# Kernel tuning notes

Measured on AMD Instinct MI355X. Metric: run time of the kernel, lower is better.

## Reference

```python
import jax, jax.numpy as jnp
import numpy as np

N = 50000      # nodes
E = 800000     # edges (before self loops)
H = 4          # heads
C_IN = 128     # input feature dim
C_HID = 64     # per-head out channels (hidden_dim == output_dim)
SLOPE = 0.2    # GATConv leaky_relu negative slope


def setup_inputs() -> dict:
    key = jax.random.key(0)
    ks = jax.random.split(key, 16)
    x = jax.random.normal(ks[0], (N, C_IN), jnp.float32)
    edge_index = jax.random.randint(ks[1], (2, E), 0, N, jnp.int32)

    def p(k, shape):
        return jax.random.normal(k, shape, jnp.float32) * 0.05

    inp = {"x": x, "edge_index": edge_index}
    in_dims = [C_IN, C_HID, C_HID]
    for i in range(3):
        inp[f"W{i+1}"] = p(ks[2 + 4 * i], (in_dims[i], H * C_HID))
        inp[f"asrc{i+1}"] = p(ks[3 + 4 * i], (H, C_HID))
        inp[f"adst{i+1}"] = p(ks[4 + 4 * i], (H, C_HID))
        inp[f"b{i+1}"] = jnp.zeros((C_HID,), jnp.float32)
    return inp


def _gat_layer(x, src, dst, W, a_s, a_d, b):
    # x: [N, F_in]; src/dst: [E'] (self loops included)
    n = x.shape[0]
    h = (x @ W).reshape(n, H, -1)                      # [N, H, C]
    alpha_src = jnp.einsum('nhc,hc->nh', h, a_s)       # att_src . h  (source side)
    alpha_dst = jnp.einsum('nhc,hc->nh', h, a_d)       # att_dst . h  (target side)
    e = jax.nn.leaky_relu(alpha_src[src] + alpha_dst[dst], SLOPE)  # [E', H]
    # scatter-softmax over incoming edges of each dst node
    m = jax.ops.segment_max(e, dst, num_segments=n)    # [N, H]
    ex = jnp.exp(e - m[dst])
    denom = jax.ops.segment_sum(ex, dst, num_segments=n)
    alpha = ex / (denom[dst] + 1e-16)                  # [E', H]
    # scatter-add aggregation of weighted source features
    out = jax.ops.segment_sum(alpha[:, :, None] * h[src], dst, num_segments=n)  # [N, H, C]
    return out.mean(axis=1) + b                        # concat=False -> head mean, + bias


def reference(x, edge_index, W1, asrc1, adst1, b1, W2, asrc2, adst2, b2,
              W3, asrc3, adst3, b3):
    n = x.shape[0]
    loops = jnp.arange(n, dtype=edge_index.dtype)      # GATConv add_self_loops=True
    src = jnp.concatenate([edge_index[0], loops])
    dst = jnp.concatenate([edge_index[1], loops])
    for W, a_s, a_d, b in ((W1, asrc1, adst1, b1),
                           (W2, asrc2, adst2, b2),
                           (W3, asrc3, adst3, b3)):
        x = jax.nn.relu(_gat_layer(x, src, dst, W, a_s, a_d, b))
    return x
```

## Files before the change

### kernel.cpp

```cpp
#include <hip/hip_runtime.h>
#include <hip/hip_bf16.h>
#include <cstddef>

#define NH 4
#define CHID 64
#define HC 256

typedef __attribute__((ext_vector_type(8))) short bf16x8;
typedef __attribute__((ext_vector_type(4))) float f32x4;


__global__ void hist_kernel(const int* __restrict__ ei, int E, int N,
                            int* __restrict__ deg) {
  int i = blockIdx.x * blockDim.x + threadIdx.x;
  int EP = E + N;
  if (i >= EP) return;
  int d = (i < E) ? ei[E + i] : (i - E);
  atomicAdd(&deg[d], 1);
}

__global__ __launch_bounds__(256) void partial_sum_kernel(const int* __restrict__ deg,
                                                          int* __restrict__ part, int n) {
  __shared__ int red[4];
  int t = threadIdx.x;
  int i = blockIdx.x * 256 + t;
  int v = (i < n) ? deg[i] : 0;
#pragma unroll
  for (int o = 32; o; o >>= 1) v += __shfl_xor(v, o, 64);
  if ((t & 63) == 0) red[t >> 6] = v;
  __syncthreads();
  if (t == 0) part[blockIdx.x] = red[0] + red[1] + red[2] + red[3];
}

__global__ __launch_bounds__(256) void scan_part_kernel(int* __restrict__ part, int nb,
                                                        int* __restrict__ row_off, int n) {
  __shared__ int s[256];
  int t = threadIdx.x;
  int v = (t < nb) ? part[t] : 0;
  s[t] = v;
  __syncthreads();
  for (int o = 1; o < 256; o <<= 1) {
    int u = (t >= o) ? s[t - o] : 0;
    __syncthreads();
    s[t] += u;
    __syncthreads();
  }
  if (t < nb) part[t] = s[t] - v;
  if (t == 255) row_off[n] = s[255];
}

__global__ __launch_bounds__(256) void row_off_kernel(const int* __restrict__ deg,
                                                      const int* __restrict__ part,
                                                      int* __restrict__ row_off, int n) {
  __shared__ int s[256];
  int t = threadIdx.x;
  int i = blockIdx.x * 256 + t;
  int v = (i < n) ? deg[i] : 0;
  s[t] = v;
  __syncthreads();
  for (int o = 1; o < 256; o <<= 1) {
    int u = (t >= o) ? s[t - o] : 0;
    __syncthreads();
    s[t] += u;
    __syncthreads();
  }
  if (i < n) row_off[i] = part[blockIdx.x] + s[t] - v;
}

__global__ void scatter_kernel(const int* __restrict__ ei, int E, int N,
                               const int* __restrict__ row_off,
                               int* __restrict__ cursor, int* __restrict__ ssrc) {
  int i = blockIdx.x * blockDim.x + threadIdx.x;
  int EP = E + N;
  if (i >= EP) {
    if (i < EP + 8) ssrc[i] = 0;
    return;
  }
  int s, d;
  if (i < E) { s = ei[i]; d = ei[E + i]; } else { s = i - E; d = s; }
  int pos = row_off[d] + atomicAdd(&cursor[d], 1);
  ssrc[pos] = s;
}


__global__ void prep_kernel(const float* __restrict__ x,
                            __hip_bfloat16* __restrict__ xb, int n4,
                            const float* __restrict__ W1, const float* __restrict__ W2,
                            const float* __restrict__ W3,
                            __hip_bfloat16* __restrict__ w1b,
                            __hip_bfloat16* __restrict__ w2b,
                            __hip_bfloat16* __restrict__ w3b) {
  int i = blockIdx.x * blockDim.x + threadIdx.x;
  if (i < n4) {
    float4 v = reinterpret_cast<const float4*>(x)[i];
    __hip_bfloat16 h[4] = {__float2bfloat16(v.x), __float2bfloat16(v.y),
                           __float2bfloat16(v.z), __float2bfloat16(v.w)};
    reinterpret_cast<uint2*>(xb)[i] = *reinterpret_cast<uint2*>(h);
    return;
  }
  int j = i - n4;
  if (j >= 65536) return;
  const float* W; __hip_bfloat16* wb; int K, base;
  if (j < 32768)      { W = W1; wb = w1b; K = 128; base = j; }
  else if (j < 49152) { W = W2; wb = w2b; K = 64;  base = j - 32768; }
  else                { W = W3; wb = w3b; K = 64;  base = j - 49152; }
  int k = base >> 8;
  int c = base & 255;
  wb[c * K + k] = __float2bfloat16(W[base]);
}


template <int K>
__global__ __launch_bounds__(256) void gemm_mfma_kernel(
    const __hip_bfloat16* __restrict__ Ab,
    const __hip_bfloat16* __restrict__ Btb,
    const float* __restrict__ a_s, const float* __restrict__ a_d,
    __hip_bfloat16* __restrict__ h, float* __restrict__ asrc_n,
    float* __restrict__ adst_n, int n_rows, int row_groups) {
  extern __shared__ char smem[];
  uint4* lds4 = reinterpret_cast<uint4*>(smem);
  constexpr int KS = K / 32;
  constexpr int S16 = (128 * K * 2) >> 4;
  constexpr int rowshift = (K == 128) ? 4 : 3;
  int ch = blockIdx.y;
  int colbase = ch * 128;

  {
    const uint4* g = reinterpret_cast<const uint4*>(Btb + (size_t)colbase * K);
    for (int c = threadIdx.x; c < S16; c += 256) {
      int row = c >> rowshift;
      lds4[c ^ (row & 7)] = g[c];
    }
  }
  __syncthreads();

  int wave = threadIdx.x >> 6;
  int lane = threadIdx.x & 63;
  int n16  = lane & 15;
  int g4   = lane >> 4;
  const bf16x8 z8 = {0, 0, 0, 0, 0, 0, 0, 0};

  for (int gg = blockIdx.x; gg < row_groups; gg += gridDim.x) {
    int row0 = gg * 64 + wave * 16;
    int xrow = row0 + n16;
    bool aval = xrow < n_rows;
    size_t xbase = (size_t)xrow * K + g4 * 8;

    bf16x8 xh[KS];
#pragma unroll
    for (int s = 0; s < KS; ++s)
      xh[s] = aval ? *reinterpret_cast<const bf16x8*>(&Ab[xbase + s * 32]) : z8;

    f32x4 acc[8];
#pragma unroll
    for (int ct = 0; ct < 8; ++ct) acc[ct] = (f32x4){0.f, 0.f, 0.f, 0.f};

#pragma unroll
    for (int ct = 0; ct < 8; ++ct) {
      int wrow = ct * 16 + n16;
#pragma unroll
      for (int s = 0; s < KS; ++s) {
        int ci = ((wrow * K + s * 32 + g4 * 8) >> 3) ^ (wrow & 7);
        bf16x8 wh = *reinterpret_cast<const bf16x8*>(&lds4[ci]);
        acc[ct] = __builtin_amdgcn_mfma_f32_16x16x32_bf16(wh, xh[s], acc[ct], 0, 0, 0);
      }
    }

    int r = row0 + n16;
    bool valid = r < n_rows;

    if (valid) {
#pragma unroll
      for (int ct = 0; ct < 8; ++ct) {
        unsigned short u[4];
#pragma unroll
        for (int i = 0; i < 4; ++i) {
          __hip_bfloat16 b = __float2bfloat16(acc[ct][i]);
          u[i] = *reinterpret_cast<unsigned short*>(&b);
        }
        *reinterpret_cast<uint2*>(&h[(size_t)r * HC + colbase + ct * 16 + g4 * 4]) =
            *reinterpret_cast<uint2*>(u);
      }
    }

    float ps[2] = {0.f, 0.f};
    float pd[2] = {0.f, 0.f};
#pragma unroll
    for (int ct = 0; ct < 8; ++ct) {
      int hh = ct >> 2;
      int col = colbase + ct * 16 + g4 * 4;
      float4 as4 = *reinterpret_cast<const float4*>(&a_s[col]);
      float4 ad4 = *reinterpret_cast<const float4*>(&a_d[col]);
      ps[hh] += acc[ct][0] * as4.x + acc[ct][1] * as4.y + acc[ct][2] * as4.z + acc[ct][3] * as4.w;
      pd[hh] += acc[ct][0] * ad4.x + acc[ct][1] * ad4.y + acc[ct][2] * ad4.z + acc[ct][3] * ad4.w;
    }
#pragma unroll
    for (int hh = 0; hh < 2; ++hh) {
      ps[hh] += __shfl_xor(ps[hh], 16, 64);
      ps[hh] += __shfl_xor(ps[hh], 32, 64);
      pd[hh] += __shfl_xor(pd[hh], 16, 64);
      pd[hh] += __shfl_xor(pd[hh], 32, 64);
    }
    if (lane < 16 && valid) {
      *reinterpret_cast<float2*>(&asrc_n[(size_t)r * NH + ch * 2]) =
          make_float2(ps[0], ps[1]);
      *reinterpret_cast<float2*>(&adst_n[(size_t)r * NH + ch * 2]) =
          make_float2(pd[0], pd[1]);
    }
  }
}


__global__ __launch_bounds__(256) void aggregate_kernel(
    const int* __restrict__ row_off, const int* __restrict__ ssrc,
    const __hip_bfloat16* __restrict__ h, const float* __restrict__ asrc_n,
    const float* __restrict__ adst_n, const float* __restrict__ bias,
    __hip_bfloat16* __restrict__ out_bf, float* __restrict__ out_f32, int n_nodes) {
  int n = (blockIdx.x * blockDim.x + threadIdx.x) >> 6;
  if (n >= n_nodes) return;
  int l    = threadIdx.x & 63;
  int slot = l >> 3;
  int cp   = l & 7;
  const char* hbase = reinterpret_cast<const char*>(h);
  const float4 z4 = make_float4(0.f, 0.f, 0.f, 0.f);
  const uint4 zu = {0, 0, 0, 0};

  int beg  = row_off[n];
  int deg  = row_off[n + 1] - beg;
  float4 adn = reinterpret_cast<const float4*>(adst_n)[n];

  float facc[32];
#pragma unroll
  for (int u = 0; u < 32; ++u) facc[u] = 0.f;
  float4 ds = z4;

  auto LOADE = [&](int j, float4& a4, float& msk, uint4* d) {
    int jj  = j + slot;
    int idx = beg + jj;
    int sv  = ssrc[idx];
    a4  = reinterpret_cast<const float4*>(asrc_n)[sv];
    msk = (jj < deg) ? 1.f : 0.f;
    const char* hp = hbase + (size_t)sv * 512 + cp * 16;
    d[0] = *reinterpret_cast<const uint4*>(hp);
    d[1] = *reinterpret_cast<const uint4*>(hp + 128);
    d[2] = *reinterpret_cast<const uint4*>(hp + 256);
    d[3] = *reinterpret_cast<const uint4*>(hp + 384);
  };

  auto PROC = [&](const float4& a4, float msk, const uint4* d) {
    float e0 = a4.x + adn.x; e0 = fmaxf(e0, 0.2f * e0);
    float e1 = a4.y + adn.y; e1 = fmaxf(e1, 0.2f * e1);
    float e2 = a4.z + adn.z; e2 = fmaxf(e2, 0.2f * e2);
    float e3 = a4.w + adn.w; e3 = fmaxf(e3, 0.2f * e3);
    float w0 = __expf(e0) * msk;
    float w1 = __expf(e1) * msk;
    float w2 = __expf(e2) * msk;
    float w3 = __expf(e3) * msk;
    ds.x += w0; ds.y += w1; ds.z += w2; ds.w += w3;
#pragma unroll
    for (int hh = 0; hh < 4; ++hh) {
      float w = (hh == 0) ? w0 : (hh == 1) ? w1 : (hh == 2) ? w2 : w3;
      uint4 dd = d[hh];
      facc[hh * 8 + 0] += w * __uint_as_float(dd.x << 16);
      facc[hh * 8 + 1] += w * __uint_as_float(dd.x & 0xffff0000u);
      facc[hh * 8 + 2] += w * __uint_as_float(dd.y << 16);
      facc[hh * 8 + 3] += w * __uint_as_float(dd.y & 0xffff0000u);
      facc[hh * 8 + 4] += w * __uint_as_float(dd.z << 16);
      facc[hh * 8 + 5] += w * __uint_as_float(dd.z & 0xffff0000u);
      facc[hh * 8 + 6] += w * __uint_as_float(dd.w << 16);
      facc[hh * 8 + 7] += w * __uint_as_float(dd.w & 0xffff0000u);
    }
  };

  float4 aA = z4, aB = z4;
  float mA = 0.f, mB = 0.f;
  uint4 dA[4] = {zu, zu, zu, zu};
  uint4 dB[4] = {zu, zu, zu, zu};

  LOADE(0, aA, mA, dA);
  for (int j = 0; j < deg; j += 16) {
    if (j + 8 < deg) LOADE(j + 8, aB, mB, dB); else mB = 0.f;
    PROC(aA, mA, dA);
    if (j + 16 < deg) LOADE(j + 16, aA, mA, dA); else mA = 0.f;
    PROC(aB, mB, dB);
  }

#pragma unroll
  for (int o = 8; o <= 32; o <<= 1) {
    ds.x += __shfl_xor(ds.x, o, 64);
    ds.y += __shfl_xor(ds.y, o, 64);
    ds.z += __shfl_xor(ds.z, o, 64);
    ds.w += __shfl_xor(ds.w, o, 64);
  }
  float iv0 = 1.f / (ds.x + 1e-16f);
  float iv1 = 1.f / (ds.y + 1e-16f);
  float iv2 = 1.f / (ds.z + 1e-16f);
  float iv3 = 1.f / (ds.w + 1e-16f);

  float v[8];
#pragma unroll
  for (int u = 0; u < 8; ++u)
    v[u] = facc[u] * iv0 + facc[8 + u] * iv1 + facc[16 + u] * iv2 + facc[24 + u] * iv3;

#pragma unroll
  for (int u = 0; u < 8; ++u) {
    v[u] += __shfl_xor(v[u], 8, 64);
    v[u] += __shfl_xor(v[u], 16, 64);
    v[u] += __shfl_xor(v[u], 32, 64);
  }

  if (slot < 2) {
    float o0 = (slot == 0) ? v[0] : v[4];
    float o1 = (slot == 0) ? v[1] : v[5];
    float o2 = (slot == 0) ? v[2] : v[6];
    float o3 = (slot == 0) ? v[3] : v[7];
    int chn = cp * 8 + slot * 4;
    float4 b4 = *reinterpret_cast<const float4*>(&bias[chn]);
    o0 = fmaxf(0.25f * o0 + b4.x, 0.f);
    o1 = fmaxf(0.25f * o1 + b4.y, 0.f);
    o2 = fmaxf(0.25f * o2 + b4.z, 0.f);
    o3 = fmaxf(0.25f * o3 + b4.w, 0.f);
    if (out_f32) {
      *reinterpret_cast<float4*>(&out_f32[(size_t)n * CHID + chn]) =
          make_float4(o0, o1, o2, o3);
    } else {
      float of[4] = {o0, o1, o2, o3};
      unsigned short b16[4];
#pragma unroll
      for (int u = 0; u < 4; ++u) {
        __hip_bfloat16 bh = __float2bfloat16(of[u]);
        b16[u] = *reinterpret_cast<unsigned short*>(&bh);
      }
      *reinterpret_cast<uint2*>(&out_bf[(size_t)n * CHID + chn]) =
          *reinterpret_cast<uint2*>(b16);
    }
  }
}


extern "C" void kernel_launch(void* const* d_in, const int* in_sizes, int n_in,
                              void* d_out, int out_size, void* d_ws, size_t ws_size,
                              hipStream_t stream) {
  const float* x   = (const float*)d_in[0];
  const int*   ei  = (const int*)d_in[1];
  const float* W1  = (const float*)d_in[2];
  const float* as1 = (const float*)d_in[3];
  const float* ad1 = (const float*)d_in[4];
  const float* b1  = (const float*)d_in[5];
  const float* W2  = (const float*)d_in[6];
  const float* as2 = (const float*)d_in[7];
  const float* ad2 = (const float*)d_in[8];
  const float* b2  = (const float*)d_in[9];
  const float* W3  = (const float*)d_in[10];
  const float* as3 = (const float*)d_in[11];
  const float* ad3 = (const float*)d_in[12];
  const float* b3  = (const float*)d_in[13];

  int N  = in_sizes[0] / 128;
  int E  = in_sizes[1] / 2;
  int EP = E + N;
  int NB = (N + 255) / 256;

  __hip_bfloat16* h    = (__hip_bfloat16*)d_ws;
  __hip_bfloat16* x1b  = h + (size_t)N * HC;
  __hip_bfloat16* xb   = x1b + (size_t)N * 128;
  __hip_bfloat16* w1b  = xb + (size_t)N * CHID;
  __hip_bfloat16* w2b  = w1b + 256 * 128;
  __hip_bfloat16* w3b  = w2b + 256 * 64;
  float* asrc_n = (float*)(w3b + 256 * 64);
  float* adst_n = asrc_n + (size_t)N * NH;
  int*   deg    = (int*)(adst_n + (size_t)N * NH);
  int*   cursor = deg + N;
  int*   row_off= cursor + N;
  int*   part   = row_off + (N + 1);
  int*   ssrc   = part + ((NB + 3) & ~3);

  hipMemsetAsync(deg, 0, sizeof(int) * (size_t)2 * N, stream);
  int eb = (EP + 8 + 255) / 256;
  hist_kernel<<<eb, 256, 0, stream>>>(ei, E, N, deg);
  partial_sum_kernel<<<NB, 256, 0, stream>>>(deg, part, N);
  scan_part_kernel<<<1, 256, 0, stream>>>(part, NB, row_off, N);
  row_off_kernel<<<NB, 256, 0, stream>>>(deg, part, row_off, N);
  scatter_kernel<<<eb, 256, 0, stream>>>(ei, E, N, row_off, cursor, ssrc);

  int n4 = N * 128 / 4;
  prep_kernel<<<(n4 + 65536 + 255) / 256, 256, 0, stream>>>(x, x1b, n4,
                                                            W1, W2, W3, w1b, w2b, w3b);

  (void)hipFuncSetAttribute(reinterpret_cast<const void*>(&gemm_mfma_kernel<128>),
                            hipFuncAttributeMaxDynamicSharedMemorySize, 65536);
  (void)hipFuncSetAttribute(reinterpret_cast<const void*>(&gemm_mfma_kernel<64>),
                            hipFuncAttributeMaxDynamicSharedMemorySize, 65536);

  int RG = (N + 63) / 64;
  dim3 ggrid(RG, 2);
  int ablocks = (N + 3) / 4;

  gemm_mfma_kernel<128><<<ggrid, 256, 32768, stream>>>(x1b, w1b, as1, ad1,
                                                       h, asrc_n, adst_n, N, RG);
  aggregate_kernel<<<ablocks, 256, 0, stream>>>(row_off, ssrc, h, asrc_n, adst_n, b1,
                                                xb, nullptr, N);
  gemm_mfma_kernel<64><<<ggrid, 256, 16384, stream>>>(xb, w2b, as2, ad2,
                                                      h, asrc_n, adst_n, N, RG);
  aggregate_kernel<<<ablocks, 256, 0, stream>>>(row_off, ssrc, h, asrc_n, adst_n, b2,
                                                xb, nullptr, N);
  gemm_mfma_kernel<64><<<ggrid, 256, 16384, stream>>>(xb, w3b, as3, ad3,
                                                      h, asrc_n, adst_n, N, RG);
  aggregate_kernel<<<ablocks, 256, 0, stream>>>(row_off, ssrc, h, asrc_n, adst_n, b3,
                                                nullptr, (float*)d_out, N);
}
```

Baseline: 367.8 us.

## Split aggregation into per-head/half slices with precomputed edge weights and combine pass

```diff
diff --git a/kernel.cpp b/kernel.cpp
--- a/kernel.cpp
+++ b/kernel.cpp
@@ -69,17 +69,19 @@
 
 __global__ void scatter_kernel(const int* __restrict__ ei, int E, int N,
                                const int* __restrict__ row_off,
-                               int* __restrict__ cursor, int* __restrict__ ssrc) {
+                               int* __restrict__ cursor, int* __restrict__ ssrc,
+                               int* __restrict__ sdst) {
   int i = blockIdx.x * blockDim.x + threadIdx.x;
   int EP = E + N;
   if (i >= EP) {
-    if (i < EP + 8) ssrc[i] = 0;
+    if (i < EP + 16) { ssrc[i] = 0; sdst[i] = 0; }
     return;
   }
   int s, d;
   if (i < E) { s = ei[i]; d = ei[E + i]; } else { s = i - E; d = s; }
   int pos = row_off[d] + atomicAdd(&cursor[d], 1);
   ssrc[pos] = s;
+  sdst[pos] = d;
 }
 
 
@@ -211,129 +213,128 @@
 }
 
 
+__global__ void edge_weight_kernel(const int* __restrict__ ssrc, const int* __restrict__ sdst,
+                                   const float* __restrict__ asrc_n,
+                                   const float* __restrict__ adst_n,
+                                   float4* __restrict__ wbuf, int EP) {
+  int i = blockIdx.x * blockDim.x + threadIdx.x;
+  if (i >= EP) {
+    if (i < EP + 16) wbuf[i] = make_float4(0.f, 0.f, 0.f, 0.f);
+    return;
+  }
+  int s = ssrc[i];
+  int d = sdst[i];
+  float4 a = reinterpret_cast<const float4*>(asrc_n)[s];
+  float4 b = reinterpret_cast<const float4*>(adst_n)[d];
+  float e0 = a.x + b.x; e0 = fmaxf(e0, 0.2f * e0);
+  float e1 = a.y + b.y; e1 = fmaxf(e1, 0.2f * e1);
+  float e2 = a.z + b.z; e2 = fmaxf(e2, 0.2f * e2);
+  float e3 = a.w + b.w; e3 = fmaxf(e3, 0.2f * e3);
+  wbuf[i] = make_float4(__expf(e0), __expf(e1), __expf(e2), __expf(e3));
+}
+
+
 __global__ __launch_bounds__(256) void aggregate_kernel(
     const int* __restrict__ row_off, const int* __restrict__ ssrc,
-    const __hip_bfloat16* __restrict__ h, const float* __restrict__ asrc_n,
-    const float* __restrict__ adst_n, const float* __restrict__ bias,
-    __hip_bfloat16* __restrict__ out_bf, float* __restrict__ out_f32, int n_nodes) {
-  int n = (blockIdx.x * blockDim.x + threadIdx.x) >> 6;
-  if (n >= n_nodes) return;
-  int l    = threadIdx.x & 63;
-  int slot = l >> 3;
-  int cp   = l & 7;
-  const char* hbase = reinterpret_cast<const char*>(h);
-  const float4 z4 = make_float4(0.f, 0.f, 0.f, 0.f);
+    const __hip_bfloat16* __restrict__ h, const float* __restrict__ wbuf4,
+    float* __restrict__ pf, int n_nodes) {
+  int bid   = blockIdx.x;
+  int slice = bid & 7;
+  int ng    = bid >> 3;
+  int head  = slice >> 1;
+  int half  = slice & 1;
+  int wave  = threadIdx.x >> 6;
+  int l     = threadIdx.x & 63;
+  int slot  = l >> 2;
+  int q     = l & 3;
+  const char* hb = reinterpret_cast<const char*>(h) + head * 128 + half * 64 + q * 16;
+  float* pfh = pf + (size_t)head * n_nodes * 64 + half * 32 + q * 8;
   const uint4 zu = {0, 0, 0, 0};
 
-  int beg  = row_off[n];
-  int deg  = row_off[n + 1] - beg;
-  float4 adn = reinterpret_cast<const float4*>(adst_n)[n];
-
-  float facc[32];
-#pragma unroll
-  for (int u = 0; u < 32; ++u) facc[u] = 0.f;
-  float4 ds = z4;
-
-  auto LOADE = [&](int j, float4& a4, float& msk, uint4* d) {
-    int jj  = j + slot;
-    int idx = beg + jj;
-    int sv  = ssrc[idx];
-    a4  = reinterpret_cast<const float4*>(asrc_n)[sv];
-    msk = (jj < deg) ? 1.f : 0.f;
-    const char* hp = hbase + (size_t)sv * 512 + cp * 16;
-    d[0] = *reinterpret_cast<const uint4*>(hp);
-    d[1] = *reinterpret_cast<const uint4*>(hp + 128);
-    d[2] = *reinterpret_cast<const uint4*>(hp + 256);
-    d[3] = *reinterpret_cast<const uint4*>(hp + 384);
-  };
-
-  auto PROC = [&](const float4& a4, float msk, const uint4* d) {
-    float e0 = a4.x + adn.x; e0 = fmaxf(e0, 0.2f * e0);
-    float e1 = a4.y + adn.y; e1 = fmaxf(e1, 0.2f * e1);
-    float e2 = a4.z + adn.z; e2 = fmaxf(e2, 0.2f * e2);
-    float e3 = a4.w + adn.w; e3 = fmaxf(e3, 0.2f * e3);
-    float w0 = __expf(e0) * msk;
-    float w1 = __expf(e1) * msk;
-    float w2 = __expf(e2) * msk;
-    float w3 = __expf(e3) * msk;
-    ds.x += w0; ds.y += w1; ds.z += w2; ds.w += w3;
-#pragma unroll
-    for (int hh = 0; hh < 4; ++hh) {
-      float w = (hh == 0) ? w0 : (hh == 1) ? w1 : (hh == 2) ? w2 : w3;
-      uint4 dd = d[hh];
-      facc[hh * 8 + 0] += w * __uint_as_float(dd.x << 16);
-      facc[hh * 8 + 1] += w * __uint_as_float(dd.x & 0xffff0000u);
-      facc[hh * 8 + 2] += w * __uint_as_float(dd.y << 16);
-      facc[hh * 8 + 3] += w * __uint_as_float(dd.y & 0xffff0000u);
-      facc[hh * 8 + 4] += w * __uint_as_float(dd.z << 16);
-      facc[hh * 8 + 5] += w * __uint_as_float(dd.z & 0xffff0000u);
-      facc[hh * 8 + 6] += w * __uint_as_float(dd.w << 16);
-      facc[hh * 8 + 7] += w * __uint_as_float(dd.w & 0xffff0000u);
-    }
-  };
-
-  float4 aA = z4, aB = z4;
-  float mA = 0.f, mB = 0.f;
-  uint4 dA[4] = {zu, zu, zu, zu};
-  uint4 dB[4] = {zu, zu, zu, zu};
-
-  LOADE(0, aA, mA, dA);
-  for (int j = 0; j < deg; j += 16) {
-    if (j + 8 < deg) LOADE(j + 8, aB, mB, dB); else mB = 0.f;
-    PROC(aA, mA, dA);
-    if (j + 16 < deg) LOADE(j + 16, aA, mA, dA); else mA = 0.f;
-    PROC(aB, mB, dB);
-  }
-
-#pragma unroll
-  for (int o = 8; o <= 32; o <<= 1) {
-    ds.x += __shfl_xor(ds.x, o, 64);
-    ds.y += __shfl_xor(ds.y, o, 64);
-    ds.z += __shfl_xor(ds.z, o, 64);
-    ds.w += __shfl_xor(ds.w, o, 64);
-  }
-  float iv0 = 1.f / (ds.x + 1e-16f);
-  float iv1 = 1.f / (ds.y + 1e-16f);
-  float iv2 = 1.f / (ds.z + 1e-16f);
-  float iv3 = 1.f / (ds.w + 1e-16f);
-
-  float v[8];
-#pragma unroll
-  for (int u = 0; u < 8; ++u)
-    v[u] = facc[u] * iv0 + facc[8 + u] * iv1 + facc[16 + u] * iv2 + facc[24 + u] * iv3;
-
-#pragma unroll
-  for (int u = 0; u < 8; ++u) {
-    v[u] += __shfl_xor(v[u], 8, 64);
-    v[u] += __shfl_xor(v[u], 16, 64);
-    v[u] += __shfl_xor(v[u], 32, 64);
-  }
-
-  if (slot < 2) {
-    float o0 = (slot == 0) ? v[0] : v[4];
-    float o1 = (slot == 0) ? v[1] : v[5];
-    float o2 = (slot == 0) ? v[2] : v[6];
-    float o3 = (slot == 0) ? v[3] : v[7];
-    int chn = cp * 8 + slot * 4;
-    float4 b4 = *reinterpret_cast<const float4*>(&bias[chn]);
-    o0 = fmaxf(0.25f * o0 + b4.x, 0.f);
-    o1 = fmaxf(0.25f * o1 + b4.y, 0.f);
-    o2 = fmaxf(0.25f * o2 + b4.z, 0.f);
-    o3 = fmaxf(0.25f * o3 + b4.w, 0.f);
-    if (out_f32) {
-      *reinterpret_cast<float4*>(&out_f32[(size_t)n * CHID + chn]) =
-          make_float4(o0, o1, o2, o3);
-    } else {
-      float of[4] = {o0, o1, o2, o3};
-      unsigned short b16[4];
-#pragma unroll
-      for (int u = 0; u < 4; ++u) {
-        __hip_bfloat16 bh = __float2bfloat16(of[u]);
-        b16[u] = *reinterpret_cast<unsigned short*>(&bh);
-      }
-      *reinterpret_cast<uint2*>(&out_bf[(size_t)n * CHID + chn]) =
-          *reinterpret_cast<uint2*>(b16);
-    }
+  for (int t = 0; t < 2; ++t) {
+    int n = ng * 8 + wave * 2 + t;
+    if (n >= n_nodes) return;
+    int beg = row_off[n];
+    int deg = row_off[n + 1] - beg;
+
+    float facc[8];
+#pragma unroll
+    for (int u = 0; u < 8; ++u) facc[u] = 0.f;
+    float dsum = 0.f;
+
+    auto LOADE = [&](int j, float& w, uint4& d) {
+      int jj  = j + slot;
+      int idx = beg + jj;
+      int sv  = ssrc[idx];
+      float wv = wbuf4[idx * 4 + head];
+      w = (jj < deg) ? wv : 0.f;
+      d = *reinterpret_cast<const uint4*>(hb + (size_t)sv * 512);
+    };
+
+    auto PROC = [&](float w, const uint4& d) {
+      dsum += w;
+      facc[0] += w * __uint_as_float(d.x << 16);
+      facc[1] += w * __uint_as_float(d.x & 0xffff0000u);
+      facc[2] += w * __uint_as_float(d.y << 16);
+      facc[3] += w * __uint_as_float(d.y & 0xffff0000u);
+      facc[4] += w * __uint_as_float(d.z << 16);
+      facc[5] += w * __uint_as_float(d.z & 0xffff0000u);
+      facc[6] += w * __uint_as_float(d.w << 16);
+      facc[7] += w * __uint_as_float(d.w & 0xffff0000u);
+    };
+
+    float wA = 0.f, wB = 0.f;
+    uint4 dA = zu, dB = zu;
+    LOADE(0, wA, dA);
+    for (int j = 0; j < deg; j += 32) {
+      if (j + 16 < deg) LOADE(j + 16, wB, dB); else wB = 0.f;
+      PROC(wA, dA);
+      if (j + 32 < deg) LOADE(j + 32, wA, dA); else wA = 0.f;
+      PROC(wB, dB);
+    }
+
+#pragma unroll
+    for (int o = 4; o <= 32; o <<= 1) dsum += __shfl_xor(dsum, o, 64);
+    float sc = 0.25f / (dsum + 1e-16f);
+#pragma unroll
+    for (int u = 0; u < 8; ++u) {
+#pragma unroll
+      for (int o = 4; o <= 32; o <<= 1) facc[u] += __shfl_xor(facc[u], o, 64);
+      facc[u] *= sc;
+    }
+
+    if (slot == 0) {
+      float* dst = &pfh[(size_t)n * 64];
+      *reinterpret_cast<float4*>(dst)     = make_float4(facc[0], facc[1], facc[2], facc[3]);
+      *reinterpret_cast<float4*>(dst + 4) = make_float4(facc[4], facc[5], facc[6], facc[7]);
+    }
+  }
+}
+
+
+__global__ void combine_kernel(const float* __restrict__ pf, const float* __restrict__ bias,
+                               __hip_bfloat16* __restrict__ out_bf,
+                               float* __restrict__ out_f32, int n_nodes) {
+  int i = blockIdx.x * blockDim.x + threadIdx.x;
+  int total = n_nodes * 16;
+  if (i >= total) return;
+  size_t stride = (size_t)n_nodes * 16;
+  const float4* p = reinterpret_cast<const float4*>(pf);
+  float4 a = p[i];
+  float4 b = p[i + stride];
+  float4 c = p[i + 2 * stride];
+  float4 d = p[i + 3 * stride];
+  float4 bs = reinterpret_cast<const float4*>(bias)[i & 15];
+  float o0 = fmaxf(a.x + b.x + c.x + d.x + bs.x, 0.f);
+  float o1 = fmaxf(a.y + b.y + c.y + d.y + bs.y, 0.f);
+  float o2 = fmaxf(a.z + b.z + c.z + d.z + bs.z, 0.f);
+  float o3 = fmaxf(a.w + b.w + c.w + d.w + bs.w, 0.f);
+  if (out_f32) {
+    reinterpret_cast<float4*>(out_f32)[i] = make_float4(o0, o1, o2, o3);
+  } else {
+    __hip_bfloat16 u[4] = {__float2bfloat16(o0), __float2bfloat16(o1),
+                           __float2bfloat16(o2), __float2bfloat16(o3)};
+    reinterpret_cast<uint2*>(out_bf)[i] = *reinterpret_cast<uint2*>(u);
   }
 }
 
@@ -369,19 +370,22 @@
   __hip_bfloat16* w3b  = w2b + 256 * 64;
   float* asrc_n = (float*)(w3b + 256 * 64);
   float* adst_n = asrc_n + (size_t)N * NH;
-  int*   deg    = (int*)(adst_n + (size_t)N * NH);
+  float* wbuf   = adst_n + (size_t)N * NH;
+  float* pf     = wbuf + (size_t)(EP + 16) * 4;
+  int*   deg    = (int*)(pf + (size_t)4 * N * CHID);
   int*   cursor = deg + N;
   int*   row_off= cursor + N;
   int*   part   = row_off + (N + 1);
   int*   ssrc   = part + ((NB + 3) & ~3);
+  int*   sdst   = ssrc + (EP + 16);
 
   hipMemsetAsync(deg, 0, sizeof(int) * (size_t)2 * N, stream);
-  int eb = (EP + 8 + 255) / 256;
+  int eb = (EP + 16 + 255) / 256;
   hist_kernel<<<eb, 256, 0, stream>>>(ei, E, N, deg);
   partial_sum_kernel<<<NB, 256, 0, stream>>>(deg, part, N);
   scan_part_kernel<<<1, 256, 0, stream>>>(part, NB, row_off, N);
   row_off_kernel<<<NB, 256, 0, stream>>>(deg, part, row_off, N);
-  scatter_kernel<<<eb, 256, 0, stream>>>(ei, E, N, row_off, cursor, ssrc);
+  scatter_kernel<<<eb, 256, 0, stream>>>(ei, E, N, row_off, cursor, ssrc, sdst);
 
   int n4 = N * 128 / 4;
   prep_kernel<<<(n4 + 65536 + 255) / 256, 256, 0, stream>>>(x, x1b, n4,
@@ -394,18 +398,25 @@
 
   int RG = (N + 63) / 64;
   dim3 ggrid(RG, 2);
-  int ablocks = (N + 3) / 4;
+  int ablocks = 8 * ((N + 7) / 8);
+  int cblocks = (N * 16 + 255) / 256;
 
   gemm_mfma_kernel<128><<<ggrid, 256, 32768, stream>>>(x1b, w1b, as1, ad1,
                                                        h, asrc_n, adst_n, N, RG);
-  aggregate_kernel<<<ablocks, 256, 0, stream>>>(row_off, ssrc, h, asrc_n, adst_n, b1,
-                                                xb, nullptr, N);
+  edge_weight_kernel<<<eb, 256, 0, stream>>>(ssrc, sdst, asrc_n, adst_n,
+                                             (float4*)wbuf, EP);
+  aggregate_kernel<<<ablocks, 256, 0, stream>>>(row_off, ssrc, h, wbuf, pf, N);
+  combine_kernel<<<cblocks, 256, 0, stream>>>(pf, b1, xb, nullptr, N);
   gemm_mfma_kernel<64><<<ggrid, 256, 16384, stream>>>(xb, w2b, as2, ad2,
                                                       h, asrc_n, adst_n, N, RG);
-  aggregate_kernel<<<ablocks, 256, 0, stream>>>(row_off, ssrc, h, asrc_n, adst_n, b2,
-                                                xb, nullptr, N);
+  edge_weight_kernel<<<eb, 256, 0, stream>>>(ssrc, sdst, asrc_n, adst_n,
+                                             (float4*)wbuf, EP);
+  aggregate_kernel<<<ablocks, 256, 0, stream>>>(row_off, ssrc, h, wbuf, pf, N);
+  combine_kernel<<<cblocks, 256, 0, stream>>>(pf, b2, xb, nullptr, N);
   gemm_mfma_kernel<64><<<ggrid, 256, 16384, stream>>>(xb, w3b, as3, ad3,
                                                       h, asrc_n, adst_n, N, RG);
-  aggregate_kernel<<<ablocks, 256, 0, stream>>>(row_off, ssrc, h, asrc_n, adst_n, b3,
-                                                nullptr, (float*)d_out, N);
-}
+  edge_weight_kernel<<<eb, 256, 0, stream>>>(ssrc, sdst, asrc_n, adst_n,
+                                             (float4*)wbuf, EP);
+  aggregate_kernel<<<ablocks, 256, 0, stream>>>(row_off, ssrc, h, wbuf, pf, N);
+  combine_kernel<<<cblocks, 256, 0, stream>>>(pf, b3, nullptr, (float*)d_out, N);
+}
```

New measurement: 673.3 us. +83.0%, slower.
